# Kernel optimization log

Measured on AMD Instinct MI355X. Metric: run time of the kernel, lower is better.

Reference implementation:

```python
import jax, jax.numpy as jnp
import numpy as np

D = 1024
B = 16
SP = 256
T = B * SP
DT_REF = 1.0
MAX_GROWTH = 0.3


def _cayley(re, im):
    A = re + 1j * im
    A = A - A.conj().T  # skew-Hermitian part
    I = jnp.eye(A.shape[0], dtype=A.dtype)
    return jnp.linalg.solve(I + A, I - A)


def _dft_basis(d):
    n = jnp.arange(d)
    k = jnp.arange(d)[:, None]
    ang = -2.0 * jnp.pi * (k * n).astype(jnp.float32) / d
    return jnp.exp(1j * ang) / jnp.sqrt(jnp.float32(d))


def _forward(x_input, h_prev_re, h_prev_im, xg_re, xg_im, flux_re, flux_im, dt,
             u_raw_re, u_raw_im, v_raw_re, v_raw_im, log_sigma, dft_weight,
             decay_re, decay_im, Wi, bi, Wo, bo, Wg, bg,
             ld, lf, law_re, law_im, base_noise, Wu1, bu1, Wu2, bu2,
             noise_re, noise_im):
    d = x_input.shape[-1]
    # ---- basis.encode ----
    V = _cayley(v_raw_re, v_raw_im)                       # [D,D] complex
    s_diag = jnp.exp(log_sigma).astype(V.dtype)
    xc = x_input.astype(jnp.complex64)
    alpha = jax.nn.sigmoid(dft_weight)
    x_tilde = (xc @ V) * s_diag * (1.0 - alpha) + (xc @ _dft_basis(d)) * alpha
    x_tilde = x_tilde[:, None, :]                          # [T,1,D]
    # ---- flux_tracker.forward_step ----
    fdecay = jax.nn.sigmoid(decay_re) + 1j * decay_im
    x_cat = jnp.concatenate([xg_re, xg_im], axis=-1)       # [B,2D]
    xin = x_cat @ Wi.T + bi
    update = xin[..., :d] + 1j * xin[..., d:]
    flux_next = (flux_re + 1j * flux_im) * fdecay + update
    s_cat = jnp.concatenate([flux_next.real, flux_next.imag], axis=-1)
    proj = s_cat @ Wo.T + bo
    source = proj[..., :d] + 1j * proj[..., d:]            # [B,D] complex
    gate = jax.nn.sigmoid(s_cat @ Wg.T + bg)               # [B,D] real
    # ---- transition operators ----
    l_re = jnp.tanh(-jnp.exp(ld) + law_re) * MAX_GROWTH
    lam = l_re + 1j * (lf + law_im)
    dt_ratio = dt / DT_REF                                 # [1]
    op_decay = jnp.exp(lam[None, :] * dt_ratio[:, None].astype(jnp.complex64))
    op_forcing = (op_decay - 1.0) / (lam[None, :] + 1e-8)
    # ---- expand source/gate over spatial ----
    bsz = source.shape[0]
    sp = x_tilde.shape[0] // bsz
    src = jnp.broadcast_to(source[:, None, None, :], (bsz, sp, 1, d)).reshape(-1, 1, d)
    g = jnp.broadcast_to(gate[:, None, None, :], (bsz, sp, 1, d)).reshape(-1, 1, d)
    forcing = x_tilde * g + src * (1.0 - g)
    h_prev = h_prev_re + 1j * h_prev_im
    h_next = h_prev * op_decay + forcing * op_forcing      # [T,1,D]
    # ---- SDE stochastic term ----
    base_var = base_noise ** 2 * jnp.expm1(2.0 * l_re * dt_ratio[:, None]) / (2.0 * l_re + 1e-8)
    base_var = jnp.maximum(base_var, 0.0)                  # [1,D]
    h_mean = h_next.mean(axis=1).real                      # [T,D]
    u = jax.nn.softplus(jax.nn.silu(h_mean @ Wu1.T + bu1) @ Wu2.T + bu2)  # [T,D]
    std = jnp.sqrt(base_var * u)[:, None, :].astype(h_next.dtype)          # [T,1,D]
    noise = (noise_re + 1j * noise_im) * jnp.sqrt(jnp.float32(0.5))
    return h_next + noise * std, flux_next


def setup_inputs() -> dict:
    key = jax.random.key(0)
    ks = jax.random.split(key, 40)
    rn = lambda i, shp, sc=1.0: jax.random.normal(ks[i], shp, jnp.float32) * sc
    q_re = jnp.linalg.qr(rn(0, (D, D)))[0]
    q_im = jnp.linalg.qr(rn(1, (D, D)))[0]
    return {
        "x_input": rn(2, (T, D)),
        "h_prev_re": rn(3, (T, 1, D)), "h_prev_im": rn(4, (T, 1, D)),
        "xg_re": rn(5, (B, D)), "xg_im": rn(6, (B, D)),
        "flux_re": rn(7, (B, D)), "flux_im": rn(8, (B, D)),
        "dt": jnp.ones((1,), jnp.float32),
        "u_raw_re": q_re * 0.1, "u_raw_im": q_im * 0.1,
        "v_raw_re": q_re.T * 0.1, "v_raw_im": q_im.T * 0.1,
        "log_sigma": jnp.zeros((D,), jnp.float32),
        "dft_weight": jnp.float32(0.2),
        "decay_re": rn(9, (D,), 0.1) - 1.0, "decay_im": rn(10, (D,), 0.1),
        "Wi": rn(11, (2 * D, 2 * D), 0.02), "bi": jnp.zeros((2 * D,), jnp.float32),
        "Wo": rn(12, (2 * D, 2 * D), 0.02), "bo": jnp.zeros((2 * D,), jnp.float32),
        "Wg": rn(13, (D, 2 * D), 0.02), "bg": jnp.zeros((D,), jnp.float32),
        "ld": rn(14, (D,), 0.5) - 2.0, "lf": rn(15, (D,), 1.0),
        "law_re": rn(16, (D,), 0.01), "law_im": rn(17, (D,), 0.01),
        "base_noise": jnp.float32(0.01),
        "Wu1": rn(18, (D // 4, D), 0.03), "bu1": jnp.zeros((D // 4,), jnp.float32),
        "Wu2": rn(19, (D, D // 4), 0.06), "bu2": jnp.zeros((D,), jnp.float32),
        "noise_re": rn(20, (T, 1, D)), "noise_im": rn(21, (T, 1, D)),
    }


def reference(x_input, h_prev_re, h_prev_im, xg_re, xg_im, flux_re, flux_im, dt,
              u_raw_re, u_raw_im, v_raw_re, v_raw_im, log_sigma, dft_weight,
              decay_re, decay_im, Wi, bi, Wo, bo, Wg, bg,
              ld, lf, law_re, law_im, base_noise, Wu1, bu1, Wu2, bu2,
              noise_re, noise_im):
    return _forward(x_input, h_prev_re, h_prev_im, xg_re, xg_im, flux_re, flux_im, dt,
                    u_raw_re, u_raw_im, v_raw_re, v_raw_im, log_sigma, dft_weight,
                    decay_re, decay_im, Wi, bi, Wo, bo, Wg, bg,
                    ld, lf, law_re, law_im, base_noise, Wu1, bu1, Wu2, bu2,
                    noise_re, noise_im)
```

## Files before the change

### kernel.cpp

```cpp
#include <hip/hip_runtime.h>
#include <cstddef>

#define TPB 256

typedef short bf8v  __attribute__((ext_vector_type(8)));
typedef float f32x4 __attribute__((ext_vector_type(4)));
typedef unsigned short u16;

#define PSZ 2048
#define PSZ2 4096
#define LSTR 40
#define BUF1 2560
#define CSTR 68
#define RTBUF 12288

static __device__ __forceinline__ u16 f2bf(float x) {
  unsigned int u = __float_as_uint(x);
  u = (u + 0x7FFFu + ((u >> 16) & 1u)) >> 16;
  return (u16)u;
}
static __device__ __forceinline__ float bf2f(u16 x) {
  return __uint_as_float(((unsigned int)x) << 16);
}
static __device__ __forceinline__ float sigmoidf_(float x) {
  return 1.0f / (1.0f + __expf(-x));
}
static __device__ __forceinline__ float spf_(float v) {
  return (v > 15.0f) ? v : __logf(1.0f + __expf(v));
}
static __device__ __forceinline__ bf8v neg8(bf8v a) {
  #pragma unroll
  for (int i = 0; i < 8; ++i) a[i] ^= (short)0x8000;
  return a;
}
static __device__ __forceinline__ void pack8(const float4& x, const float4& y,
                                             u16* dst) {
  unsigned int* d = (unsigned int*)dst;
  d[0] = ((unsigned)f2bf(x.y) << 16) | f2bf(x.x);
  d[1] = ((unsigned)f2bf(x.w) << 16) | f2bf(x.z);
  d[2] = ((unsigned)f2bf(y.y) << 16) | f2bf(y.x);
  d[3] = ((unsigned)f2bf(y.w) << 16) | f2bf(y.z);
}
static __device__ __forceinline__ uint2 packbf4(float a, float b, float c, float d) {
  uint2 r;
  r.x = ((unsigned)f2bf(b) << 16) | f2bf(a);
  r.y = ((unsigned)f2bf(d) << 16) | f2bf(c);
  return r;
}
static __device__ __forceinline__ void gload16(const u16* g, u16* l) {
  __builtin_amdgcn_global_load_lds((const __attribute__((address_space(1))) void*)g,
                                   (__attribute__((address_space(3))) void*)l,
                                   16, 0, 0);
}
static __device__ __forceinline__ bf8v fragld(const u16* plane, int r, int kq) {
  int kb = (kq << 4) ^ (((r >> 1) & 3) << 4);
  return *(const bf8v*)(plane + r * 32 + (kb >> 1));
}
static __device__ __forceinline__ bf8v fragld2(const u16* plane, int r, int kq, int s) {
  int ch = ((s << 2) + kq) ^ (r & 7);
  return *(const bf8v*)(plane + r * 64 + (ch << 3));
}
static __device__ __forceinline__ int swz8(int flat, int T) {
  return (flat & 7) * (T >> 3) + (flat >> 3);
}

#define WAITV(n) asm volatile("s_waitcnt vmcnt(" #n ")" ::: "memory")

__global__ __launch_bounds__(TPB) void build_a_k(
    const float* __restrict__ vre, const float* __restrict__ vim,
    u16* __restrict__ Ar, u16* __restrict__ Ai,
    u16* __restrict__ Nr, u16* __restrict__ Ni)
{
  int idx = blockIdx.x * TPB + threadIdx.x;
  int i = idx >> 10, j = idx & 1023;
  float ar = vre[idx] - vre[j * 1024 + i];
  float ai = vim[idx] + vim[j * 1024 + i];
  float dg = (i == j) ? 1.0f : 0.0f;
  Ar[idx] = f2bf(ar);       Ai[idx] = f2bf(ai);
  Nr[idx] = f2bf(dg - ar);  Ni[idx] = f2bf(-ai);
}

#define CG_VARS                                                              \
  int lane = tid & 63;                                                       \
  int wr = (tid >> 7) & 1, wc = (tid >> 6) & 1;                              \
  int lr8_ = ((tid & 63) >> 3) + ((tid >> 6) << 4);                          \
  int ks2_ = (((lane & 7) ^ (lane >> 3)) << 3);                              \
  u16* Lw_ = lds + ((tid >> 6) << 10);                                       \
  f32x4 accR[2][2] = {};                                                     \
  f32x4 accI[2][2] = {};

#define CG_STAGE(buf, k0, PAr, PAi, PBr, PBi)                                \
  { u16* Lb = Lw_ + (buf) * (4 * PSZ2);                                      \
    gload16((PAr) + (size_t)(bm + lr8_) * 1024 + (k0) + ks2_,     Lb + 0 * PSZ2);       \
    gload16((PAr) + (size_t)(bm + lr8_ + 8) * 1024 + (k0) + ks2_, Lb + 0 * PSZ2 + 512); \
    gload16((PAi) + (size_t)(bm + lr8_) * 1024 + (k0) + ks2_,     Lb + 1 * PSZ2);       \
    gload16((PAi) + (size_t)(bm + lr8_ + 8) * 1024 + (k0) + ks2_, Lb + 1 * PSZ2 + 512); \
    gload16((PBr) + (size_t)(bn + lr8_) * 1024 + (k0) + ks2_,     Lb + 2 * PSZ2);       \
    gload16((PBr) + (size_t)(bn + lr8_ + 8) * 1024 + (k0) + ks2_, Lb + 2 * PSZ2 + 512); \
    gload16((PBi) + (size_t)(bn + lr8_) * 1024 + (k0) + ks2_,     Lb + 3 * PSZ2);       \
    gload16((PBi) + (size_t)(bn + lr8_ + 8) * 1024 + (k0) + ks2_, Lb + 3 * PSZ2 + 512); }

#define CG_FRAGS(buf, s)                                                     \
  const u16* L = lds + (buf) * (4 * PSZ2);                                   \
  int rA = wr * 32 + (lane & 15);                                            \
  int rB = wc * 32 + (lane & 15);                                            \
  int kq = lane >> 4;                                                        \
  bf8v ar[2], ai[2], br[2], bi[2];                                           \
  ar[0] = fragld2(L + 0 * PSZ2, rA, kq, s);  ar[1] = fragld2(L + 0 * PSZ2, rA + 16, kq, s); \
  ai[0] = fragld2(L + 1 * PSZ2, rA, kq, s);  ai[1] = fragld2(L + 1 * PSZ2, rA + 16, kq, s); \
  br[0] = fragld2(L + 2 * PSZ2, rB, kq, s);  br[1] = fragld2(L + 2 * PSZ2, rB + 16, kq, s); \
  bi[0] = fragld2(L + 3 * PSZ2, rB, kq, s);  bi[1] = fragld2(L + 3 * PSZ2, rB + 16, kq, s);

#define CG_MFMA_BNEG1                                                        \
  { bf8v nbi[2] = { neg8(bi[0]), neg8(bi[1]) };                              \
    _Pragma("unroll")                                                        \
    for (int mf = 0; mf < 2; ++mf)                                           \
      _Pragma("unroll")                                                      \
      for (int nf = 0; nf < 2; ++nf) {                                       \
        accR[mf][nf] = __builtin_amdgcn_mfma_f32_16x16x32_bf16(ar[mf], br[nf],  accR[mf][nf], 0, 0, 0); \
        accR[mf][nf] = __builtin_amdgcn_mfma_f32_16x16x32_bf16(ai[mf], bi[nf],  accR[mf][nf], 0, 0, 0); \
        accI[mf][nf] = __builtin_amdgcn_mfma_f32_16x16x32_bf16(ar[mf], nbi[nf], accI[mf][nf], 0, 0, 0); \
        accI[mf][nf] = __builtin_amdgcn_mfma_f32_16x16x32_bf16(ai[mf], br[nf],  accI[mf][nf], 0, 0, 0); \
      } }

#define CG_PIPELINE(MFMA_OP, PAr, PAi, PBr, PBi)                             \
  CG_STAGE(0, 0, PAr, PAi, PBr, PBi);                                        \
  _Pragma("unroll 1")                                                        \
  for (int t = 0; t < 16; ++t) {                                             \
    int bufc = t & 1;                                                        \
    if (t + 1 < 16) { CG_STAGE(bufc ^ 1, (t + 1) * 64, PAr, PAi, PBr, PBi);  \
                      WAITV(8); }                                            \
    else            { WAITV(0); }                                            \
    __builtin_amdgcn_sched_barrier(0);                                       \
    __builtin_amdgcn_s_barrier();                                            \
    __builtin_amdgcn_s_setprio(1);                                           \
    { CG_FRAGS(bufc, 0) MFMA_OP }                                            \
    { CG_FRAGS(bufc, 1) MFMA_OP }                                            \
    __builtin_amdgcn_s_setprio(0);                                           \
    __builtin_amdgcn_sched_barrier(0);                                       \
    __builtin_amdgcn_s_barrier();                                            \
  }

#define CGRT_VARS                                                            \
  int lane = tid & 63;                                                       \
  int wv = tid >> 6;                                                         \
  int wr = wv >> 1, wc = wv & 1;                                             \
  int ln8 = lane >> 3;                                                       \
  int ks2_ = (((lane & 7) ^ ln8) << 3);                                      \
  f32x4 accR[2] = {};                                                        \
  f32x4 accI[2] = {};

#define CGRT_STAGE(buf, k0, PAr, PAi, PBr, PBi)                              \
  { u16* Lb = lds + (buf) * RTBUF;                                           \
    _Pragma("unroll")                                                        \
    for (int j = 0; j < 6; ++j) {                                            \
      int idx = wv * 6 + j;                                                  \
      const u16* src; int row; int doff;                                     \
      if (idx < 16) {                                                        \
        int pl = idx >> 3, gr = idx & 7;                                     \
        src = pl ? (PAi) : (PAr);                                            \
        row = bm + gr * 8 + ln8;                                             \
        doff = pl * 4096 + gr * 512;                                         \
      } else {                                                               \
        int i2 = idx - 16;                                                   \
        int pl = i2 >> 2, gr = i2 & 3;                                       \
        src = pl ? (PBi) : (PBr);                                            \
        row = bn + gr * 8 + ln8;                                             \
        doff = 8192 + pl * 2048 + gr * 512;                                  \
      }                                                                      \
      gload16(src + (size_t)row * 1024 + (k0) + ks2_, Lb + doff);            \
    } }

#define CGRT_FRAGS(buf, s)                                                   \
  const u16* L = lds + (buf) * RTBUF;                                        \
  int rA = wr * 32 + (lane & 15);                                            \
  int rB = wc * 16 + (lane & 15);                                            \
  int kq = lane >> 4;                                                        \
  bf8v ar[2], ai[2], br1, bi1;                                               \
  ar[0] = fragld2(L, rA, kq, s);          ar[1] = fragld2(L, rA + 16, kq, s);          \
  ai[0] = fragld2(L + 4096, rA, kq, s);   ai[1] = fragld2(L + 4096, rA + 16, kq, s);   \
  br1 = fragld2(L + 8192, rB, kq, s);                                        \
  bi1 = fragld2(L + 10240, rB, kq, s);

#define CGRT_MFMA_BNEG0                                                      \
  { bf8v nbr = neg8(br1);                                                    \
    bf8v nbi = neg8(bi1);                                                    \
    _Pragma("unroll")                                                        \
    for (int mf = 0; mf < 2; ++mf) {                                         \
      accR[mf] = __builtin_amdgcn_mfma_f32_16x16x32_bf16(ar[mf], nbr, accR[mf], 0, 0, 0); \
      accR[mf] = __builtin_amdgcn_mfma_f32_16x16x32_bf16(ai[mf], nbi, accR[mf], 0, 0, 0); \
      accI[mf] = __builtin_amdgcn_mfma_f32_16x16x32_bf16(ar[mf], bi1, accI[mf], 0, 0, 0); \
      accI[mf] = __builtin_amdgcn_mfma_f32_16x16x32_bf16(ai[mf], nbr, accI[mf], 0, 0, 0); \
    } }

#define CGRT_MFMA_BNEG1                                                      \
  { bf8v nbi = neg8(bi1);                                                    \
    _Pragma("unroll")                                                        \
    for (int mf = 0; mf < 2; ++mf) {                                         \
      accR[mf] = __builtin_amdgcn_mfma_f32_16x16x32_bf16(ar[mf], br1, accR[mf], 0, 0, 0); \
      accR[mf] = __builtin_amdgcn_mfma_f32_16x16x32_bf16(ai[mf], bi1, accR[mf], 0, 0, 0); \
      accI[mf] = __builtin_amdgcn_mfma_f32_16x16x32_bf16(ar[mf], nbi, accI[mf], 0, 0, 0); \
      accI[mf] = __builtin_amdgcn_mfma_f32_16x16x32_bf16(ai[mf], br1, accI[mf], 0, 0, 0); \
    } }

#define CGRT_PIPELINE(MFMA_OP, PAr, PAi, PBr, PBi)                           \
  CGRT_STAGE(0, 0, PAr, PAi, PBr, PBi);                                      \
  _Pragma("unroll 1")                                                        \
  for (int t = 0; t < 16; ++t) {                                             \
    int bufc = t & 1;                                                        \
    if (t + 1 < 16) { CGRT_STAGE(bufc ^ 1, (t + 1) * 64, PAr, PAi, PBr, PBi);\
                      WAITV(6); }                                            \
    else            { WAITV(0); }                                            \
    __builtin_amdgcn_sched_barrier(0);                                       \
    __builtin_amdgcn_s_barrier();                                            \
    __builtin_amdgcn_s_setprio(1);                                           \
    { CGRT_FRAGS(bufc, 0) MFMA_OP }                                          \
    { CGRT_FRAGS(bufc, 1) MFMA_OP }                                          \
    __builtin_amdgcn_s_setprio(0);                                           \
    __builtin_amdgcn_sched_barrier(0);                                       \
    __builtin_amdgcn_s_barrier();                                            \
  }

__global__ __launch_bounds__(TPB) void d2_k(
    const u16* __restrict__ Apr, const u16* __restrict__ Api,
    u16* __restrict__ A2r, u16* __restrict__ A2i,
    const float* __restrict__ X, const float* __restrict__ Wu1,
    const float* __restrict__ Wu2,
    const float* __restrict__ ld, const float* __restrict__ lf,
    const float* __restrict__ law_re, const float* __restrict__ law_im,
    const float* __restrict__ dt, const float* __restrict__ base_noise,
    u16* __restrict__ Xb, u16* __restrict__ Wu1b, u16* __restrict__ Wu2b,
    float* __restrict__ od_re, float* __restrict__ od_im,
    float* __restrict__ of_re, float* __restrict__ of_im,
    float* __restrict__ bvar,
    const float* __restrict__ xg_re, const float* __restrict__ xg_im,
    const float* __restrict__ Wi, float* __restrict__ PpI)
{
  __shared__ __align__(16) u16 lds[2 * RTBUF];
  int tid = threadIdx.x;
  int bx = blockIdx.x;
  if (bx < 512) {
    int flat = swz8(bx, 512);
    int bm = (flat >> 5) * 64, bn = (flat & 31) * 32;
    CGRT_VARS
    CGRT_PIPELINE(CGRT_MFMA_BNEG0, Apr, Api, Apr, Api)
    #pragma unroll
    for (int mf = 0; mf < 2; ++mf) {
      int col = bn + wc * 16 + (lane & 15);
      #pragma unroll
      for (int r = 0; r < 4; ++r) {
        int rowg = bm + wr * 32 + mf * 16 + (lane >> 4) * 4 + r;
        size_t o = (size_t)rowg * 1024 + col;
        A2r[o] = f2bf(accR[mf][r]);
        A2i[o] = f2bf(accI[mf][r]);
      }
    }
  } else if (bx < 2816) {
    int e = ((bx - 512) * TPB + tid) << 3;
    const float* src;
    u16* dst;
    if (e < 4194304)       { src = X + e;               dst = Xb + e; }
    else if (e < 4456448)  { src = Wu1 + (e - 4194304); dst = Wu1b + (e - 4194304); }
    else                   { src = Wu2 + (e - 4456448); dst = Wu2b + (e - 4456448); }
    float4 a = *(const float4*)src;
    float4 b = *(const float4*)(src + 4);
    u16 tmp[8];
    pack8(a, b, tmp);
    *(bf8v*)dst = *(bf8v*)tmp;
  } else if (bx < 2820) {
    int d = (bx - 2816) * TPB + tid;
    float dtr = dt[0];
    float lre = tanhf(-expf(ld[d]) + law_re[d]) * 0.3f;
    float lim = lf[d] + law_im[d];
    float er = expf(lre * dtr);
    float sn, cs;
    sincosf(lim * dtr, &sn, &cs);
    float odr = er * cs, odi = er * sn;
    od_re[d] = odr;  od_im[d] = odi;
    float numr = odr - 1.0f, numi = odi;
    float denr = lre + 1e-8f, deni = lim;
    float inv = 1.0f / (denr * denr + deni * deni);
    of_re[d] = (numr * denr + numi * deni) * inv;
    of_im[d] = (numi * denr - numr * deni) * inv;
    float bn2 = base_noise[0];
    float bv = bn2 * bn2 * expm1f(2.0f * lre * dtr) / (2.0f * lre + 1e-8f);
    bvar[d] = fmaxf(bv, 0.0f);
  } else {
    int id = bx - 2820;
    int c0 = (id & 31) * 64;
    int kbase = (id >> 5) * 256;
    int lane = tid & 63;
    int w = tid >> 6;
    int row = tid >> 2, kq = (tid & 3) << 3;

    f32x4 acc = {};
    float4 pb0, pb1;
    u16* sl = lds;

    auto gload = [&](int k0) {
      const float* p = Wi + (size_t)(c0 + row) * 2048 + k0 + kq;
      pb0 = *(const float4*)p; pb1 = *(const float4*)(p + 4);
    };
    auto stolds = [&](int buf) {
      pack8(pb0, pb1, sl + buf * BUF1 + row * LSTR + kq);
    };
    auto compute = [&](int buf, int k0) {
      int ar = lane & 15;
      int ko = (lane >> 4) * 8;
      const float* ap = (k0 < 1024) ? (xg_re + (size_t)ar * 1024 + k0 + ko)
                                    : (xg_im + (size_t)ar * 1024 + k0 + ko - 1024);
      float4 a0 = *(const float4*)ap, a1 = *(const float4*)(ap + 4);
      u16 abuf[8];
      pack8(a0, a1, abuf);
      bf8v af = *(bf8v*)abuf;
      bf8v bfr = *(const bf8v*)(sl + buf * BUF1 + (w * 16 + (lane & 15)) * LSTR + ko);
      acc = __builtin_amdgcn_mfma_f32_16x16x32_bf16(af, bfr, acc, 0, 0, 0);
    };

    gload(kbase); stolds(0); __syncthreads();
    int cur = 0;
    for (int t = 0; t < 8; ++t) {
      int k0 = kbase + t * 32;
      if (t < 7) gload(k0 + 32);
      compute(cur, k0);
      if (t < 7) stolds(cur ^ 1);
      __syncthreads();
      cur ^= 1;
    }
    int c = c0 + w * 16 + (lane & 15);
    #pragma unroll
    for (int r = 0; r < 4; ++r) {
      int rr = (lane >> 4) * 4 + r;
      PpI[((size_t)(id >> 5) * 16 + rr) * 2048 + c] = acc[r];
    }
  }
}

__global__ __launch_bounds__(TPB) void d3_k(
    const u16* __restrict__ A2r, const u16* __restrict__ A2i,
    const u16* __restrict__ Nr2, const u16* __restrict__ Ni2,
    u16* __restrict__ A4r, u16* __restrict__ A4i,
    u16* __restrict__ T1r, u16* __restrict__ T1i,
    const float* __restrict__ PpI, const float* __restrict__ bi,
    float* __restrict__ xin)
{
  __shared__ __align__(16) u16 lds[2 * 4 * PSZ2];
  int tid = threadIdx.x;
  int bx = blockIdx.x;
  if (bx < 512) {
    int flat = swz8(bx, 512);
    int z = flat >> 8;
    int t8 = flat & 255;
    int bm = (t8 >> 4) * 64, bn = (t8 & 15) * 64;
    const u16* Apr = z ? Nr2 : A2r;
    const u16* Api = z ? Ni2 : A2i;
    u16* Cr16 = z ? T1r : A4r;
    u16* Ci16 = z ? T1i : A4i;
    CG_VARS
    CG_PIPELINE(CG_MFMA_BNEG1, Apr, Api, A2r, A2i)
    #pragma unroll
    for (int mf = 0; mf < 2; ++mf)
      #pragma unroll
      for (int nf = 0; nf < 2; ++nf) {
        int col = bn + wc * 32 + nf * 16 + (lane & 15);
        #pragma unroll
        for (int r = 0; r < 4; ++r) {
          int rowg = bm + wr * 32 + mf * 16 + (lane >> 4) * 4 + r;
          size_t o = (size_t)rowg * 1024 + col;
          float vr = accR[mf][nf][r], vi = accI[mf][nf][r];
          if (z) { vr += bf2f(Nr2[o]); vi += bf2f(Ni2[o]); }
          Cr16[o] = f2bf(vr);
          Ci16[o] = f2bf(vi);
        }
      }
  } else {
    int idx = (bx - 512) * TPB + tid;
    int c = idx & 2047;
    float v = bi[c];
    #pragma unroll
    for (int s = 0; s < 8; ++s) v += PpI[(size_t)s * 32768 + idx];
    xin[idx] = v;
  }
}

__global__ __launch_bounds__(TPB) void d4_k(
    const u16* __restrict__ T1r, const u16* __restrict__ T1i,
    const u16* __restrict__ A4r, const u16* __restrict__ A4i,
    const float* __restrict__ log_sigma, const float* __restrict__ dft_weight,
    u16* __restrict__ Mtr, u16* __restrict__ Mti,
    const float* __restrict__ xin,
    const float* __restrict__ flux_re, const float* __restrict__ flux_im,
    const float* __restrict__ decay_re, const float* __restrict__ decay_im,
    float* __restrict__ FNr, float* __restrict__ FNi,
    float* __restrict__ out1)
{
  __shared__ __align__(16) u16 lds[2 * RTBUF];
  int tid = threadIdx.x;
  int bx = blockIdx.x;
  if (bx < 512) {
    int flat = swz8(bx, 512);
    int bm = (flat >> 5) * 64, bn = (flat & 31) * 32;
    CGRT_VARS
    CGRT_PIPELINE(CGRT_MFMA_BNEG1, T1r, T1i, A4r, A4i)

    u16* mtLr = lds;
    u16* mtLi = lds + 2304;
    __syncthreads();
    {
      float alpha = sigmoidf_(dft_weight[0]);
      const float isq = 0.03125f * alpha;
      #pragma unroll
      for (int mf = 0; mf < 2; ++mf) {
        int dl = wc * 16 + (lane & 15);
        int dgl = bn + dl;
        float w1 = expf(log_sigma[dgl]) * (1.0f - alpha);
        #pragma unroll
        for (int r = 0; r < 4; ++r) {
          int kl = wr * 32 + mf * 16 + (lane >> 4) * 4 + r;
          int kgl = bm + kl;
          size_t o = (size_t)kgl * 1024 + dgl;
          float dg = (kgl == dgl) ? 1.0f : 0.0f;
          float vr = 2.0f * accR[mf][r] + 2.0f * bf2f(T1r[o]) - dg;
          float vi = 2.0f * accI[mf][r] + 2.0f * bf2f(T1i[o]);
          int mm = (kgl * dgl) & 1023;
          float ang = -6.283185307179586f * (float)mm * (1.0f / 1024.0f);
          float sn, cs;
          sincosf(ang, &sn, &cs);
          mtLr[dl * 72 + kl] = f2bf(vr * w1 + cs * isq);
          mtLi[dl * 72 + kl] = f2bf(vi * w1 + sn * isq);
        }
      }
    }
    __syncthreads();
    {
      int dl = tid >> 3, kl0 = (tid & 7) * 8;
      size_t o = (size_t)(bn + dl) * 1024 + bm + kl0;
      *(uint4*)(Mtr + o) = *(uint4*)(mtLr + dl * 72 + kl0);
      *(uint4*)(Mti + o) = *(uint4*)(mtLi + dl * 72 + kl0);
    }
  } else {
    int idx = (bx - 512) * TPB + tid;
    int b = idx >> 10, d = idx & 1023;
    float fdr = sigmoidf_(decay_re[d]);
    float fdi = decay_im[d];
    float fr = flux_re[idx], fi = flux_im[idx];
    float ur = xin[b * 2048 + d], ui = xin[b * 2048 + 1024 + d];
    float nr = fr * fdr - fi * fdi + ur;
    float ni = fr * fdi + fi * fdr + ui;
    FNr[idx] = nr;  FNi[idx] = ni;
    out1[idx] = nr;
  }
}

__global__ __launch_bounds__(TPB) void sgemm16_wog_k(
    const float* __restrict__ A0, const float* __restrict__ A1,
    const float* __restrict__ Wo, const float* __restrict__ Wg,
    float* __restrict__ PpO, float* __restrict__ PpG)
{
  __shared__ __align__(16) u16 lds[2 * BUF1];
  int tid = threadIdx.x;
  int bx = blockIdx.x;
  const float* Bw = (bx < 32) ? Wo : Wg;
  float* Pp = (bx < 32) ? PpO : PpG;
  int N = (bx < 32) ? 2048 : 1024;
  int c0 = ((bx < 32) ? bx : (bx - 32)) * 64;
  int kbase = blockIdx.y * 256;
  int lane = tid & 63;
  int w = tid >> 6;
  int row = tid >> 2, kq = (tid & 3) << 3;

  f32x4 acc = {};
  float4 pb0, pb1;

  auto gload = [&](int k0) {
    const float* p = Bw + (size_t)(c0 + row) * 2048 + k0 + kq;
    pb0 = *(const float4*)p; pb1 = *(const float4*)(p + 4);
  };
  auto stolds = [&](int buf) {
    pack8(pb0, pb1, lds + buf * BUF1 + row * LSTR + kq);
  };
  auto compute = [&](int buf, int k0) {
    int ar = lane & 15;
    int ko = (lane >> 4) * 8;
    const float* ap = (k0 < 1024) ? (A0 + (size_t)ar * 1024 + k0 + ko)
                                  : (A1 + (size_t)ar * 1024 + k0 + ko - 1024);
    float4 a0 = *(const float4*)ap, a1 = *(const float4*)(ap + 4);
    u16 abuf[8];
    pack8(a0, a1, abuf);
    bf8v af = *(bf8v*)abuf;
    const u16* L = lds + buf * BUF1;
    bf8v bfr = *(const bf8v*)(L + (w * 16 + (lane & 15)) * LSTR + ko);
    acc = __builtin_amdgcn_mfma_f32_16x16x32_bf16(af, bfr, acc, 0, 0, 0);
  };

  gload(kbase); stolds(0); __syncthreads();
  int cur = 0;
  for (int t = 0; t < 8; ++t) {
    int k0 = kbase + t * 32;
    if (t < 7) gload(k0 + 32);
    compute(cur, k0);
    if (t < 7) stolds(cur ^ 1);
    __syncthreads();
    cur ^= 1;
  }

  int c = c0 + w * 16 + (lane & 15);
  #pragma unroll
  for (int r = 0; r < 4; ++r) {
    int rr = (lane >> 4) * 4 + r;
    Pp[((size_t)blockIdx.y * 16 + rr) * N + c] = acc[r];
  }
}

__global__ __launch_bounds__(TPB) void red16_wog_k(
    const float* __restrict__ PpO, const float* __restrict__ PpG,
    const float* __restrict__ bo, const float* __restrict__ bg,
    float* __restrict__ proj, float* __restrict__ gate)
{
  int idx = blockIdx.x * TPB + threadIdx.x;
  if (idx < 32768) {
    int c = idx & 2047;
    float v = bo[c];
    #pragma unroll
    for (int s = 0; s < 8; ++s) v += PpO[(size_t)s * 32768 + idx];
    proj[idx] = v;
  } else {
    int j = idx - 32768;
    int c = j & 1023;
    float v = bg[c];
    #pragma unroll
    for (int s = 0; s < 8; ++s) v += PpG[(size_t)s * 16384 + j];
    gate[j] = sigmoidf_(v);
  }
}

__global__ __launch_bounds__(TPB) void xmh_nt_k(
    const u16* __restrict__ Xb,
    const u16* __restrict__ Mtr, const u16* __restrict__ Mti,
    const float* __restrict__ gate, const float* __restrict__ proj,
    const float* __restrict__ od_re, const float* __restrict__ od_im,
    const float* __restrict__ of_re, const float* __restrict__ of_im,
    const float* __restrict__ hp_re, const float* __restrict__ hp_im,
    u16* __restrict__ Hrb)
{
  __shared__ __align__(16) u16 lds[2 * 16384];
  int flat = swz8(blockIdx.x, 512);
  int bm = (flat >> 4) * 128, bn = (flat & 15) * 64;
  int tid = threadIdx.x;
  int lane = tid & 63;
  int w = tid >> 6;
  int wr = w >> 1, wc = w & 1;
  int ln8 = lane >> 3;
  int ks2_ = (((lane & 7) ^ ln8) << 3);

  f32x4 accR[4][2] = {};
  f32x4 accI[4][2] = {};

#define XM_STAGE(buf, k0)                                                    \
  { u16* Lb = lds + (buf) * 16384;                                           \
    _Pragma("unroll")                                                        \
    for (int g = 0; g < 4; ++g)                                              \
      gload16(Xb + (size_t)(bm + w * 32 + g * 8 + ln8) * 1024 + (k0) + ks2_, \
              Lb + (w * 32 + g * 8) * 64);                                   \
    _Pragma("unroll")                                                        \
    for (int g = 0; g < 2; ++g) {                                            \
      gload16(Mtr + (size_t)(bn + w * 16 + g * 8 + ln8) * 1024 + (k0) + ks2_,\
              Lb + 8192 + (w * 16 + g * 8) * 64);                            \
      gload16(Mti + (size_t)(bn + w * 16 + g * 8 + ln8) * 1024 + (k0) + ks2_,\
              Lb + 12288 + (w * 16 + g * 8) * 64);                           \
    } }
#define XM_COMPUTE(buf, s)                                                   \
  { const u16* L = lds + (buf) * 16384;                                      \
    int kq = lane >> 4;                                                      \
    bf8v a[4], br[2], bi[2];                                                 \
    _Pragma("unroll")                                                        \
    for (int mf = 0; mf < 4; ++mf)                                           \
      a[mf] = fragld2(L, wr * 64 + mf * 16 + (lane & 15), kq, s);            \
    _Pragma("unroll")                                                        \
    for (int nf = 0; nf < 2; ++nf) {                                         \
      br[nf] = fragld2(L + 8192,  wc * 32 + nf * 16 + (lane & 15), kq, s);   \
      bi[nf] = fragld2(L + 12288, wc * 32 + nf * 16 + (lane & 15), kq, s);   \
    }                                                                        \
    _Pragma("unroll")                                                        \
    for (int mf = 0; mf < 4; ++mf)                                           \
      _Pragma("unroll")                                                      \
      for (int nf = 0; nf < 2; ++nf) {                                       \
        accR[mf][nf] = __builtin_amdgcn_mfma_f32_16x16x32_bf16(a[mf], br[nf], accR[mf][nf], 0, 0, 0); \
        accI[mf][nf] = __builtin_amdgcn_mfma_f32_16x16x32_bf16(a[mf], bi[nf], accI[mf][nf], 0, 0, 0); \
      } }

  XM_STAGE(0, 0);
  #pragma unroll 1
  for (int t = 0; t < 16; ++t) {
    int bufc = t & 1;
    if (t + 1 < 16) { XM_STAGE(bufc ^ 1, (t + 1) * 64); WAITV(8); }
    else            { WAITV(0); }
    __builtin_amdgcn_sched_barrier(0);
    __builtin_amdgcn_s_barrier();
    __builtin_amdgcn_s_setprio(1);
    XM_COMPUTE(bufc, 0)
    XM_COMPUTE(bufc, 1)
    __builtin_amdgcn_s_setprio(0);
    __builtin_amdgcn_sched_barrier(0);
    __builtin_amdgcn_s_barrier();
  }

  #pragma unroll
  for (int mf = 0; mf < 4; ++mf)
    #pragma unroll
    for (int nf = 0; nf < 2; ++nf) {
      int c = bn + wc * 32 + nf * 16 + (lane & 15);
      #pragma unroll
      for (int r = 0; r < 4; ++r) {
        int t = bm + wr * 64 + mf * 16 + (lane >> 4) * 4 + r;
        int b = t >> 8;
        float g  = gate[b * 1024 + c];
        float sr = proj[b * 2048 + c];
        float si = proj[b * 2048 + 1024 + c];
        float fr = accR[mf][nf][r] * g + sr * (1.0f - g);
        float fi = accI[mf][nf][r] * g + si * (1.0f - g);
        float odr = od_re[c], odi = od_im[c];
        float ofr = of_re[c], ofi = of_im[c];
        size_t off = (size_t)t * 1024 + c;
        float pr = hp_re[off], pi = hp_im[off];
        Hrb[off] = f2bf(pr * odr - pi * odi + fr * ofr - fi * ofi);
      }
    }
}

template<int KI, int EPI>
__global__ __launch_bounds__(TPB) void rgemm_nt_k(
    const u16* __restrict__ A, const u16* __restrict__ B,
    const float* __restrict__ bias,
    u16* __restrict__ C16, int nbxl, int total,
    const u16* __restrict__ HrbF, const float* __restrict__ nre,
    const float* __restrict__ bvarp, float* __restrict__ outp)
{
  __shared__ __align__(16) u16 lds[3 * 2 * PSZ];
  const int K = KI * 32;
  int tid = threadIdx.x;
  int flat = swz8(blockIdx.x, total);
  int bm = (flat >> nbxl) * 64;
  int bn = (flat & ((1 << nbxl) - 1)) * 64;
  const int N = 64 << nbxl;
  int lane = tid & 63;
  int wr = (tid >> 7) & 1, wc = (tid >> 6) & 1;
  int lr_ = ((tid & 63) >> 2) + ((tid >> 6) << 4);
  int ks_ = (((tid & 3) ^ ((tid >> 3) & 3)) << 3);
  u16* Lw_ = lds + ((tid >> 6) << 9);

  f32x4 acc[2][2] = {};

#define RG_STAGE(buf, k0)                                                    \
  { u16* Lb = Lw_ + (buf) * (2 * PSZ);                                       \
    gload16(A + (size_t)(bm + lr_) * K + (k0) + ks_, Lb + 0 * PSZ);          \
    gload16(B + (size_t)(bn + lr_) * K + (k0) + ks_, Lb + 1 * PSZ); }
#define RG_COMPUTE(buf)                                                      \
  { const u16* L = lds + (buf) * (2 * PSZ);                                  \
    int rA = wr * 32 + (lane & 15);                                          \
    int rB = wc * 32 + (lane & 15);                                          \
    int kq = lane >> 4;                                                      \
    bf8v a[2], b[2];                                                         \
    a[0] = fragld(L + 0 * PSZ, rA, kq);  a[1] = fragld(L + 0 * PSZ, rA + 16, kq); \
    b[0] = fragld(L + 1 * PSZ, rB, kq);  b[1] = fragld(L + 1 * PSZ, rB + 16, kq); \
    _Pragma("unroll")                                                        \
    for (int mf = 0; mf < 2; ++mf)                                           \
      _Pragma("unroll")                                                      \
      for (int nf = 0; nf < 2; ++nf)                                         \
        acc[mf][nf] = __builtin_amdgcn_mfma_f32_16x16x32_bf16(a[mf], b[nf], acc[mf][nf], 0, 0, 0); }

  RG_STAGE(0, 0);
  RG_STAGE(1, 32);
  #pragma unroll 1
  for (int t = 0; t < KI; ++t) {
    int bufc = t % 3;
    if (t + 2 < KI) { RG_STAGE((t + 2) % 3, (t + 2) * 32); }
    if (t + 2 < KI)      { WAITV(4); }
    else if (t + 1 < KI) { WAITV(2); }
    else                 { WAITV(0); }
    __builtin_amdgcn_sched_barrier(0);
    __builtin_amdgcn_s_barrier();
    __builtin_amdgcn_s_setprio(1);
    RG_COMPUTE(bufc)
    __builtin_amdgcn_s_setprio(0);
    __builtin_amdgcn_sched_barrier(0);
    __builtin_amdgcn_s_barrier();
  }

  if constexpr (EPI == 0) {
    #pragma unroll
    for (int mf = 0; mf < 2; ++mf)
      #pragma unroll
      for (int nf = 0; nf < 2; ++nf) {
        int c = bn + wc * 32 + nf * 16 + (lane & 15);
        #pragma unroll
        for (int r = 0; r < 4; ++r) {
          int t = bm + wr * 32 + mf * 16 + (lane >> 4) * 4 + r;
          float v = acc[mf][nf][r] + bias[c];
          v = v * sigmoidf_(v);
          C16[(size_t)t * N + c] = f2bf(v);
        }
      }
  } else {
    float* ct = (float*)lds;
    __syncthreads();
    #pragma unroll
    for (int mf = 0; mf < 2; ++mf)
      #pragma unroll
      for (int nf = 0; nf < 2; ++nf) {
        int rbase = wr * 32 + mf * 16 + (lane >> 4) * 4;
        int cc = wc * 32 + nf * 16 + (lane & 15);
        #pragma unroll
        for (int r = 0; r < 4; ++r)
          ct[(rbase + r) * CSTR + cc] = acc[mf][nf][r];
      }
    __syncthreads();
    int w = tid >> 6, l = tid & 63;
    int lcol = (l & 15) * 4;
    const float s2 = 0.7071067811865476f;
    #pragma unroll
    for (int p = 0; p < 4; ++p) {
      int lrow = w * 16 + p * 4 + (l >> 4);
      int t = bm + lrow;
      int c = bn + lcol;
      float4 v4 = *(float4*)&ct[lrow * CSTR + lcol];
      float4 bi4 = *(const float4*)(bias + c);
      float u0 = spf_(v4.x + bi4.x);
      float u1 = spf_(v4.y + bi4.y);
      float u2 = spf_(v4.z + bi4.z);
      float u3 = spf_(v4.w + bi4.w);
      size_t off = (size_t)t * 1024 + c;
      uint2 hb2 = *(const uint2*)(HrbF + off);
      float4 nr4 = *(const float4*)(nre + off);
      float4 bv4 = *(const float4*)(bvarp + c);
      float4 o;
      o.x = bf2f((u16)(hb2.x & 0xFFFF)) + nr4.x * sqrtf(bv4.x * u0) * s2;
      o.y = bf2f((u16)(hb2.x >> 16))    + nr4.y * sqrtf(bv4.y * u1) * s2;
      o.z = bf2f((u16)(hb2.y & 0xFFFF)) + nr4.z * sqrtf(bv4.z * u2) * s2;
      o.w = bf2f((u16)(hb2.y >> 16))    + nr4.w * sqrtf(bv4.w * u3) * s2;
      *(float4*)(outp + off) = o;
    }
  }
}

extern "C" void kernel_launch(void* const* d_in, const int* in_sizes, int n_in,
                              void* d_out, int out_size, void* d_ws, size_t ws_size,
                              hipStream_t stream) {
  (void)in_sizes; (void)n_in; (void)out_size;

  const float* x_input    = (const float*)d_in[0];
  const float* h_prev_re  = (const float*)d_in[1];
  const float* h_prev_im  = (const float*)d_in[2];
  const float* xg_re      = (const float*)d_in[3];
  const float* xg_im      = (const float*)d_in[4];
  const float* flux_re    = (const float*)d_in[5];
  const float* flux_im    = (const float*)d_in[6];
  const float* dt         = (const float*)d_in[7];
  const float* v_raw_re   = (const float*)d_in[10];
  const float* v_raw_im   = (const float*)d_in[11];
  const float* log_sigma  = (const float*)d_in[12];
  const float* dft_weight = (const float*)d_in[13];
  const float* decay_re   = (const float*)d_in[14];
  const float* decay_im   = (const float*)d_in[15];
  const float* Wi_in      = (const float*)d_in[16];
  const float* bi         = (const float*)d_in[17];
  const float* Wo         = (const float*)d_in[18];
  const float* bo         = (const float*)d_in[19];
  const float* Wg         = (const float*)d_in[20];
  const float* bg         = (const float*)d_in[21];
  const float* ld         = (const float*)d_in[22];
  const float* lf         = (const float*)d_in[23];
  const float* law_re     = (const float*)d_in[24];
  const float* law_im     = (const float*)d_in[25];
  const float* base_noise = (const float*)d_in[26];
  const float* Wu1        = (const float*)d_in[27];
  const float* bu1        = (const float*)d_in[28];
  const float* Wu2        = (const float*)d_in[29];
  const float* bu2        = (const float*)d_in[30];
  const float* noise_re   = (const float*)d_in[31];

  const size_t PL16 = 1024ull * 1024ull;
  if (ws_size < 16 * PL16 * 2) return;

  u16* P = (u16*)d_ws;
  u16* Ar  = P + 0 * PL16;   u16* Ai  = P + 1 * PL16;
  u16* Nr  = P + 2 * PL16;   u16* Ni  = P + 3 * PL16;
  u16* A2r = P + 4 * PL16;   u16* A2i = P + 5 * PL16;
  u16* A4r = P + 6 * PL16;   u16* A4i = P + 7 * PL16;
  u16* T1r = P + 8 * PL16;   u16* T1i = P + 9 * PL16;
  u16* Mtr = P + 2 * PL16;   u16* Mti = P + 3 * PL16;
  u16* Xb  = P + 10 * PL16;
  u16* Hrb = P + 4 * PL16;
  float* PpO = (float*)(P + 0 * PL16);
  float* PpG = PpO + 262144;
  float* PpI = (float*)(P + 14 * PL16);
  u16* mlp1b = P + 14 * PL16;
  u16* Wu1b  = P + 15 * PL16;
  u16* Wu2b  = Wu1b + 262144;
  float* sm  = (float*)(P + 15 * PL16 + 524288);
  float* xin  = sm;
  float* proj = xin + 32768;
  float* FNr  = proj + 32768;
  float* FNi  = FNr + 16384;
  float* gate = FNi + 16384;
  float* od_re = gate + 16384;
  float* od_im = od_re + 1024;
  float* of_re = od_im + 1024;
  float* of_im = of_re + 1024;
  float* bvar  = of_im + 1024;

  float* out0f = (float*)d_out;
  float* out1f = out0f + (size_t)4096 * 1024;

  build_a_k<<<4096, TPB, 0, stream>>>(v_raw_re, v_raw_im, Ar, Ai, Nr, Ni);
  d2_k<<<3076, TPB, 0, stream>>>(Ar, Ai, A2r, A2i,
                                 x_input, Wu1, Wu2,
                                 ld, lf, law_re, law_im, dt, base_noise,
                                 Xb, Wu1b, Wu2b,
                                 od_re, od_im, of_re, of_im, bvar,
                                 xg_re, xg_im, Wi_in, PpI);
  d3_k<<<640, TPB, 0, stream>>>(A2r, A2i, Nr, Ni, A4r, A4i, T1r, T1i,
                                PpI, bi, xin);
  d4_k<<<576, TPB, 0, stream>>>(T1r, T1i, A4r, A4i, log_sigma, dft_weight,
                                Mtr, Mti,
                                xin, flux_re, flux_im, decay_re, decay_im,
                                FNr, FNi, out1f);
  sgemm16_wog_k<<<dim3(48, 8), TPB, 0, stream>>>(FNr, FNi, Wo, Wg, PpO, PpG);
  red16_wog_k<<<192, TPB, 0, stream>>>(PpO, PpG, bo, bg, proj, gate);
  xmh_nt_k<<<512, TPB, 0, stream>>>(Xb, Mtr, Mti, gate, proj,
                                    od_re, od_im, of_re, of_im,
                                    h_prev_re, h_prev_im, Hrb);
  rgemm_nt_k<32, 0><<<256, TPB, 0, stream>>>(Hrb, Wu1b, bu1, mlp1b, 2, 256,
                                             nullptr, nullptr, nullptr, nullptr);
  rgemm_nt_k<8, 2><<<1024, TPB, 0, stream>>>(mlp1b, Wu2b, bu2, nullptr, 4, 1024,
                                             Hrb, noise_re, bvar, out0f);
}
```

Measured before the change: 128.5 us.

## Fuse flux update into d3 and Wo/Wg projection GEMM into d4

The flux-update elementwise work now runs in d3's spare blocks and reduces the PpI partials directly, so the xin intermediate buffer is gone. The split-K Wo/Wg projection GEMM moves from its own kernel into extra blocks of d4, running alongside the Mt construction tiles. This removes one kernel launch and a global round-trip through xin, and lets the small GEMM overlap the larger d4 work. The cost is a heterogeneous d4 grid that may need more registers or LDS per block and schedules unevenly.

```diff
diff --git a/kernel.cpp b/kernel.cpp
--- a/kernel.cpp
+++ b/kernel.cpp
@@ -342,7 +342,10 @@
     u16* __restrict__ A4r, u16* __restrict__ A4i,
     u16* __restrict__ T1r, u16* __restrict__ T1i,
     const float* __restrict__ PpI, const float* __restrict__ bi,
-    float* __restrict__ xin)
+    const float* __restrict__ flux_re, const float* __restrict__ flux_im,
+    const float* __restrict__ decay_re, const float* __restrict__ decay_im,
+    float* __restrict__ FNr, float* __restrict__ FNi,
+    float* __restrict__ out1)
 {
   __shared__ __align__(16) u16 lds[2 * 4 * PSZ2];
   int tid = threadIdx.x;
@@ -375,11 +378,21 @@
       }
   } else {
     int idx = (bx - 512) * TPB + tid;
-    int c = idx & 2047;
-    float v = bi[c];
-    #pragma unroll
-    for (int s = 0; s < 8; ++s) v += PpI[(size_t)s * 32768 + idx];
-    xin[idx] = v;
+    int b = idx >> 10, d = idx & 1023;
+    float ur = bi[d];
+    float ui = bi[1024 + d];
+    #pragma unroll
+    for (int s = 0; s < 8; ++s) {
+      ur += PpI[(size_t)s * 32768 + b * 2048 + d];
+      ui += PpI[(size_t)s * 32768 + b * 2048 + 1024 + d];
+    }
+    float fdr = sigmoidf_(decay_re[d]);
+    float fdi = decay_im[d];
+    float fr = flux_re[idx], fi = flux_im[idx];
+    float nr = fr * fdr - fi * fdi + ur;
+    float ni = fr * fdi + fi * fdr + ui;
+    FNr[idx] = nr;  FNi[idx] = ni;
+    out1[idx] = nr;
   }
 }
 
@@ -388,11 +401,9 @@
     const u16* __restrict__ A4r, const u16* __restrict__ A4i,
     const float* __restrict__ log_sigma, const float* __restrict__ dft_weight,
     u16* __restrict__ Mtr, u16* __restrict__ Mti,
-    const float* __restrict__ xin,
-    const float* __restrict__ flux_re, const float* __restrict__ flux_im,
-    const float* __restrict__ decay_re, const float* __restrict__ decay_im,
-    float* __restrict__ FNr, float* __restrict__ FNi,
-    float* __restrict__ out1)
+    const float* __restrict__ FNr, const float* __restrict__ FNi,
+    const float* __restrict__ Wo, const float* __restrict__ Wg,
+    float* __restrict__ PpO, float* __restrict__ PpG)
 {
   __shared__ __align__(16) u16 lds[2 * RTBUF];
   int tid = threadIdx.x;
@@ -439,76 +450,58 @@
       *(uint4*)(Mti + o) = *(uint4*)(mtLi + dl * 72 + kl0);
     }
   } else {
-    int idx = (bx - 512) * TPB + tid;
-    int b = idx >> 10, d = idx & 1023;
-    float fdr = sigmoidf_(decay_re[d]);
-    float fdi = decay_im[d];
-    float fr = flux_re[idx], fi = flux_im[idx];
-    float ur = xin[b * 2048 + d], ui = xin[b * 2048 + 1024 + d];
-    float nr = fr * fdr - fi * fdi + ur;
-    float ni = fr * fdi + fi * fdr + ui;
-    FNr[idx] = nr;  FNi[idx] = ni;
-    out1[idx] = nr;
-  }
-}
-
-__global__ __launch_bounds__(TPB) void sgemm16_wog_k(
-    const float* __restrict__ A0, const float* __restrict__ A1,
-    const float* __restrict__ Wo, const float* __restrict__ Wg,
-    float* __restrict__ PpO, float* __restrict__ PpG)
-{
-  __shared__ __align__(16) u16 lds[2 * BUF1];
-  int tid = threadIdx.x;
-  int bx = blockIdx.x;
-  const float* Bw = (bx < 32) ? Wo : Wg;
-  float* Pp = (bx < 32) ? PpO : PpG;
-  int N = (bx < 32) ? 2048 : 1024;
-  int c0 = ((bx < 32) ? bx : (bx - 32)) * 64;
-  int kbase = blockIdx.y * 256;
-  int lane = tid & 63;
-  int w = tid >> 6;
-  int row = tid >> 2, kq = (tid & 3) << 3;
-
-  f32x4 acc = {};
-  float4 pb0, pb1;
-
-  auto gload = [&](int k0) {
-    const float* p = Bw + (size_t)(c0 + row) * 2048 + k0 + kq;
-    pb0 = *(const float4*)p; pb1 = *(const float4*)(p + 4);
-  };
-  auto stolds = [&](int buf) {
-    pack8(pb0, pb1, lds + buf * BUF1 + row * LSTR + kq);
-  };
-  auto compute = [&](int buf, int k0) {
-    int ar = lane & 15;
-    int ko = (lane >> 4) * 8;
-    const float* ap = (k0 < 1024) ? (A0 + (size_t)ar * 1024 + k0 + ko)
-                                  : (A1 + (size_t)ar * 1024 + k0 + ko - 1024);
-    float4 a0 = *(const float4*)ap, a1 = *(const float4*)(ap + 4);
-    u16 abuf[8];
-    pack8(a0, a1, abuf);
-    bf8v af = *(bf8v*)abuf;
-    const u16* L = lds + buf * BUF1;
-    bf8v bfr = *(const bf8v*)(L + (w * 16 + (lane & 15)) * LSTR + ko);
-    acc = __builtin_amdgcn_mfma_f32_16x16x32_bf16(af, bfr, acc, 0, 0, 0);
-  };
-
-  gload(kbase); stolds(0); __syncthreads();
-  int cur = 0;
-  for (int t = 0; t < 8; ++t) {
-    int k0 = kbase + t * 32;
-    if (t < 7) gload(k0 + 32);
-    compute(cur, k0);
-    if (t < 7) stolds(cur ^ 1);
-    __syncthreads();
-    cur ^= 1;
-  }
-
-  int c = c0 + w * 16 + (lane & 15);
-  #pragma unroll
-  for (int r = 0; r < 4; ++r) {
-    int rr = (lane >> 4) * 4 + r;
-    Pp[((size_t)blockIdx.y * 16 + rr) * N + c] = acc[r];
+    int id = bx - 512;
+    int cb = id % 48;
+    int ky = id / 48;
+    const float* Bw = (cb < 32) ? Wo : Wg;
+    float* Pp = (cb < 32) ? PpO : PpG;
+    int N = (cb < 32) ? 2048 : 1024;
+    int c0 = ((cb < 32) ? cb : (cb - 32)) * 64;
+    int kbase = ky * 256;
+    int lane = tid & 63;
+    int w = tid >> 6;
+    int row = tid >> 2, kq = (tid & 3) << 3;
+
+    f32x4 acc = {};
+    float4 pb0, pb1;
+    u16* sl = lds;
+
+    auto gload = [&](int k0) {
+      const float* p = Bw + (size_t)(c0 + row) * 2048 + k0 + kq;
+      pb0 = *(const float4*)p; pb1 = *(const float4*)(p + 4);
+    };
+    auto stolds = [&](int buf) {
+      pack8(pb0, pb1, sl + buf * BUF1 + row * LSTR + kq);
+    };
+    auto compute = [&](int buf, int k0) {
+      int ar = lane & 15;
+      int ko = (lane >> 4) * 8;
+      const float* ap = (k0 < 1024) ? (FNr + (size_t)ar * 1024 + k0 + ko)
+                                    : (FNi + (size_t)ar * 1024 + k0 + ko - 1024);
+      float4 a0 = *(const float4*)ap, a1 = *(const float4*)(ap + 4);
+      u16 abuf[8];
+      pack8(a0, a1, abuf);
+      bf8v af = *(bf8v*)abuf;
+      bf8v bfr = *(const bf8v*)(sl + buf * BUF1 + (w * 16 + (lane & 15)) * LSTR + ko);
+      acc = __builtin_amdgcn_mfma_f32_16x16x32_bf16(af, bfr, acc, 0, 0, 0);
+    };
+
+    gload(kbase); stolds(0); __syncthreads();
+    int cur = 0;
+    for (int t = 0; t < 8; ++t) {
+      int k0 = kbase + t * 32;
+      if (t < 7) gload(k0 + 32);
+      compute(cur, k0);
+      if (t < 7) stolds(cur ^ 1);
+      __syncthreads();
+      cur ^= 1;
+    }
+    int c = c0 + w * 16 + (lane & 15);
+    #pragma unroll
+    for (int r = 0; r < 4; ++r) {
+      int rr = (lane >> 4) * 4 + r;
+      Pp[((size_t)ky * 16 + rr) * N + c] = acc[r];
+    }
   }
 }
 
@@ -798,8 +791,7 @@
   u16* Wu1b  = P + 15 * PL16;
   u16* Wu2b  = Wu1b + 262144;
   float* sm  = (float*)(P + 15 * PL16 + 524288);
-  float* xin  = sm;
-  float* proj = xin + 32768;
+  float* proj = sm;
   float* FNr  = proj + 32768;
   float* FNi  = FNr + 16384;
   float* gate = FNi + 16384;
@@ -819,13 +811,12 @@
                                  Xb, Wu1b, Wu2b,
                                  od_re, od_im, of_re, of_im, bvar,
                                  xg_re, xg_im, Wi_in, PpI);
-  d3_k<<<640, TPB, 0, stream>>>(A2r, A2i, Nr, Ni, A4r, A4i, T1r, T1i,
-                                PpI, bi, xin);
-  d4_k<<<576, TPB, 0, stream>>>(T1r, T1i, A4r, A4i, log_sigma, dft_weight,
+  d3_k<<<576, TPB, 0, stream>>>(A2r, A2i, Nr, Ni, A4r, A4i, T1r, T1i,
+                                PpI, bi, flux_re, flux_im, decay_re, decay_im,
+                                FNr, FNi, out1f);
+  d4_k<<<896, TPB, 0, stream>>>(T1r, T1i, A4r, A4i, log_sigma, dft_weight,
                                 Mtr, Mti,
-                                xin, flux_re, flux_im, decay_re, decay_im,
-                                FNr, FNi, out1f);
-  sgemm16_wog_k<<<dim3(48, 8), TPB, 0, stream>>>(FNr, FNi, Wo, Wg, PpO, PpG);
+                                FNr, FNi, Wo, Wg, PpO, PpG);
   red16_wog_k<<<192, TPB, 0, stream>>>(PpO, PpG, bo, bg, proj, gate);
   xmh_nt_k<<<512, TPB, 0, stream>>>(Xb, Mtr, Mti, gate, proj,
                                     od_re, od_im, of_re, of_im,
```

After: 122.3 us. 4.8% less time.
